# Kernel tuning notes

Hardware: AMD Instinct MI355X
Metric: run time of the kernel (lower is better)

## Reference

```python
import jax, jax.numpy as jnp
import numpy as np
import math

ALPHA_MIN = math.exp(-1.0 / 5.0)   # ~0.8187
ALPHA_MAX = math.exp(-1.0 / 25.0)  # ~0.9608
THRESHOLD = 1.0


def setup_inputs() -> dict:
    key = jax.random.key(0)
    k1, k2, k3, k4, k5 = jax.random.split(key, 5)
    B, T, I, H = 32, 2048, 256, 512
    x = jax.random.normal(k1, (B, T, I), dtype=jnp.float32)
    # Linear weight, kaiming-ish scale
    W = jax.random.normal(k2, (H, I), dtype=jnp.float32) * (1.0 / np.sqrt(I))
    # alpha ~ U[exp(-1/5), exp(-1/25)] as in nn.init.uniform_
    alpha = ALPHA_MIN + jax.random.uniform(k3, (H,), dtype=jnp.float32) * (ALPHA_MAX - ALPHA_MIN)
    # initial membrane potential / spike state (torch.rand in _lif_cell)
    u0 = jax.random.uniform(k4, (B, H), dtype=jnp.float32)
    s0 = jax.random.uniform(k5, (B, H), dtype=jnp.float32)
    return {"x": x, "W": W, "alpha": alpha, "u0": u0, "s0": s0}


def reference(x, W, alpha, u0, s0):
    # clamp alpha to its admissible range (lif_feature has no 'NoClamp')
    alpha = jnp.clip(alpha, ALPHA_MIN, ALPHA_MAX)
    b = 1.0 - alpha  # lif_feature has no 'B'

    # feedforward projection: [B, T, H]
    Wx = jnp.einsum('bti,hi->bth', x, W)

    def step(carry, wx_t):
        ut, st = carry
        ut = alpha * (ut - st) + b * wx_t          # leaky integrate + soft reset
        st = (ut - THRESHOLD > 0).astype(ut.dtype)  # heaviside spike
        return (ut, st), st

    # scan over time: Wx -> [T, B, H]
    _, s = jax.lax.scan(step, (u0, s0), jnp.swapaxes(Wx, 0, 1))
    return jnp.swapaxes(s, 0, 1)  # [B, T, H]
```

## Files before the change

kernel.cpp:

```cpp
#include <hip/hip_runtime.h>
#include <hip/hip_bf16.h>

#define ALPHA_MIN 0.8187307530779818f
#define ALPHA_MAX 0.9607894391523232f

typedef _Float16 f16;
typedef _Float16 f16x8 __attribute__((ext_vector_type(8)));
typedef float f32x16 __attribute__((ext_vector_type(16)));

#define LDSTRIDE 40

__global__ __launch_bounds__(256, 2) void gemm_fused(
    const float* __restrict__ X,
    const float* __restrict__ W,
    float* __restrict__ C,
    int M, int N, int K)
{
    __shared__ f16 Ah[2][128 * LDSTRIDE];
    __shared__ f16 Al[2][128 * LDSTRIDE];
    __shared__ f16 Bh[2][128 * LDSTRIDE];
    __shared__ f16 Bl[2][128 * LDSTRIDE];

    const int tid = threadIdx.x;
    const int mt = blockIdx.x >> 2;
    const int nt = blockIdx.x & 3;
    const int m0 = mt * 128, n0 = nt * 128;

    const int lane = tid & 63;
    const int wv   = tid >> 6;
    const int wm   = wv & 1;
    const int wn   = wv >> 1;
    const int fm   = lane & 31;
    const int fq   = lane >> 5;

    const int srow = tid >> 2;
    const int sc8  = tid & 3;

    const float* px0 = X + (size_t)(m0 + srow)      * K + sc8 * 8;
    const float* px1 = X + (size_t)(m0 + srow + 64) * K + sc8 * 8;
    const float* pw0 = W + (size_t)(n0 + srow)      * K + sc8 * 8;
    const float* pw1 = W + (size_t)(n0 + srow + 64) * K + sc8 * 8;

    f32x16 accH[2][2], accL[2][2];
#pragma unroll
    for (int i = 0; i < 2; ++i)
#pragma unroll
        for (int j = 0; j < 2; ++j)
#pragma unroll
            for (int e = 0; e < 16; ++e) { accH[i][j][e] = 0.0f; accL[i][j][e] = 0.0f; }

    float4 t[2][4];

    auto issue_loads = [&](int kt) {
        const int o = kt * 32;
        t[0][0] = *(const float4*)(px0 + o);
        t[0][1] = *(const float4*)(px0 + o + 4);
        t[0][2] = *(const float4*)(pw0 + o);
        t[0][3] = *(const float4*)(pw0 + o + 4);
        t[1][0] = *(const float4*)(px1 + o);
        t[1][1] = *(const float4*)(px1 + o + 4);
        t[1][2] = *(const float4*)(pw1 + o);
        t[1][3] = *(const float4*)(pw1 + o + 4);
    };

    auto write_lds = [&](int buf) {
#pragma unroll
        for (int i = 0; i < 2; ++i) {
            const int off = (srow + 64 * i) * LDSTRIDE + sc8 * 8;
            const float vx[8] = {t[i][0].x, t[i][0].y, t[i][0].z, t[i][0].w,
                                 t[i][1].x, t[i][1].y, t[i][1].z, t[i][1].w};
            const float vw[8] = {t[i][2].x, t[i][2].y, t[i][2].z, t[i][2].w,
                                 t[i][3].x, t[i][3].y, t[i][3].z, t[i][3].w};
            f16x8 xh, xl, wh, wl;
#pragma unroll
            for (int j = 0; j < 8; ++j) {
                const f16 hx = (f16)vx[j];
                xh[j] = hx; xl[j] = (f16)((vx[j] - (float)hx) * 2048.0f);
                const f16 hw = (f16)vw[j];
                wh[j] = hw; wl[j] = (f16)((vw[j] - (float)hw) * 2048.0f);
            }
            *(f16x8*)&Ah[buf][off] = xh;
            *(f16x8*)&Al[buf][off] = xl;
            *(f16x8*)&Bh[buf][off] = wh;
            *(f16x8*)&Bl[buf][off] = wl;
        }
    };

    const int KT = K / 32;
    issue_loads(0);
    write_lds(0);
    __syncthreads();

    for (int kt = 0; kt < KT; ++kt) {
        const int cur = kt & 1;
        if (kt + 1 < KT) issue_loads(kt + 1);

#pragma unroll
        for (int ks = 0; ks < 2; ++ks) {
            f16x8 af[2][2], bf[2][2];
#pragma unroll
            for (int mb = 0; mb < 2; ++mb) {
                const int ro = (wm * 64 + mb * 32 + fm) * LDSTRIDE + ks * 16 + fq * 8;
                af[mb][0] = *(const f16x8*)&Ah[cur][ro];
                af[mb][1] = *(const f16x8*)&Al[cur][ro];
            }
#pragma unroll
            for (int nb = 0; nb < 2; ++nb) {
                const int ro = (wn * 64 + nb * 32 + fm) * LDSTRIDE + ks * 16 + fq * 8;
                bf[nb][0] = *(const f16x8*)&Bh[cur][ro];
                bf[nb][1] = *(const f16x8*)&Bl[cur][ro];
            }
#pragma unroll
            for (int mb = 0; mb < 2; ++mb)
#pragma unroll
                for (int nb = 0; nb < 2; ++nb) {
                    accH[mb][nb] = __builtin_amdgcn_mfma_f32_32x32x16_f16(af[mb][0], bf[nb][0], accH[mb][nb], 0, 0, 0);
                    accL[mb][nb] = __builtin_amdgcn_mfma_f32_32x32x16_f16(af[mb][0], bf[nb][1], accL[mb][nb], 0, 0, 0);
                    accL[mb][nb] = __builtin_amdgcn_mfma_f32_32x32x16_f16(af[mb][1], bf[nb][0], accL[mb][nb], 0, 0, 0);
                }
        }

        if (kt + 1 < KT) write_lds(cur ^ 1);
        __syncthreads();
    }

#pragma unroll
    for (int mb = 0; mb < 2; ++mb)
#pragma unroll
        for (int nb = 0; nb < 2; ++nb) {
            const int col   = n0 + wn * 64 + nb * 32 + fm;
            const int rbase = m0 + wm * 64 + mb * 32 + 4 * fq;
#pragma unroll
            for (int g = 0; g < 4; ++g)
#pragma unroll
                for (int r = 0; r < 4; ++r) {
                    const int row = rbase + 8 * g + r;
                    C[(size_t)row * N + col] = accH[mb][nb][4 * g + r]
                                             + accL[mb][nb][4 * g + r] * (1.0f / 2048.0f);
                }
        }
}

#define SU 64

__global__ __launch_bounds__(64) void lif_scan2(
    const float* __restrict__ wx,
    float* __restrict__ out,
    const float* __restrict__ alpha,
    const float* __restrict__ u0,
    const float* __restrict__ s0,
    int T, int H)
{
    const int chain = blockIdx.x * 64 + threadIdx.x;
    const int h = chain % H;
    const int b = chain / H;

    float a = alpha[h];
    a = fminf(fmaxf(a, ALPHA_MIN), ALPHA_MAX);
    const float bb = 1.0f - a;

    float u = u0[chain];
    float s = s0[chain];

    const float* src = wx + (size_t)b * T * H + h;
    float* dst = out + (size_t)b * T * H + h;

    float w0[SU], w1[SU];
#pragma unroll
    for (int j = 0; j < SU; ++j) w0[j] = src[(size_t)j * H];

    const int NC = T / SU;
    for (int c = 0; c < NC; c += 2) {
#pragma unroll
        for (int j = 0; j < SU; ++j) w1[j] = src[(size_t)((c + 1) * SU + j) * H];
#pragma unroll
        for (int j = 0; j < SU; ++j) {
            u = fmaf(a, u - s, bb * w0[j]);
            s = (u > 1.0f) ? 1.0f : 0.0f;
            __builtin_nontemporal_store(s, &dst[(size_t)(c * SU + j) * H]);
        }
        if (c + 2 < NC) {
#pragma unroll
            for (int j = 0; j < SU; ++j) w0[j] = src[(size_t)((c + 2) * SU + j) * H];
        }
#pragma unroll
        for (int j = 0; j < SU; ++j) {
            u = fmaf(a, u - s, bb * w1[j]);
            s = (u > 1.0f) ? 1.0f : 0.0f;
            __builtin_nontemporal_store(s, &dst[(size_t)((c + 1) * SU + j) * H]);
        }
    }
}

__global__ __launch_bounds__(64) void lif_scan_inplace(
    float* __restrict__ buf, const float* __restrict__ alpha,
    const float* __restrict__ u0, const float* __restrict__ s0, int T, int H)
{
    const int chain = blockIdx.x * 64 + threadIdx.x;
    const int h = chain % H;
    const int b = chain / H;
    float a = alpha[h];
    a = fminf(fmaxf(a, ALPHA_MIN), ALPHA_MAX);
    const float bb = 1.0f - a;
    float u = u0[chain], s = s0[chain];
    float* base = buf + (size_t)b * T * H + h;
    for (int t0 = 0; t0 < T; t0 += 32) {
        float w[32];
#pragma unroll
        for (int j = 0; j < 32; ++j) w[j] = base[(size_t)(t0 + j) * H];
#pragma unroll
        for (int j = 0; j < 32; ++j) {
            u = fmaf(a, u - s, bb * w[j]);
            s = (u > 1.0f) ? 1.0f : 0.0f;
            base[(size_t)(t0 + j) * H] = s;
        }
    }
}

extern "C" void kernel_launch(void* const* d_in, const int* in_sizes, int n_in,
                              void* d_out, int out_size, void* d_ws, size_t ws_size,
                              hipStream_t stream) {
    const float* x     = (const float*)d_in[0];
    const float* W     = (const float*)d_in[1];
    const float* alpha = (const float*)d_in[2];
    const float* u0    = (const float*)d_in[3];
    const float* s0    = (const float*)d_in[4];
    float* out = (float*)d_out;

    const int H = in_sizes[2];
    const int I = in_sizes[1] / H;
    const int B = in_sizes[3] / H;
    const int T = in_sizes[0] / (B * I);
    const int M = B * T;

    const size_t szWx = (size_t)M * H * sizeof(float);

    if (ws_size >= szWx) {
        float* Wx = (float*)d_ws;
        gemm_fused<<<(M / 128) * (H / 128), 256, 0, stream>>>(x, W, Wx, M, H, I);
        lif_scan2<<<(B * H) / 64, 64, 0, stream>>>(Wx, out, alpha, u0, s0, T, H);
    } else {
        gemm_fused<<<(M / 128) * (H / 128), 256, 0, stream>>>(x, W, out, M, H, I);
        lif_scan_inplace<<<(B * H) / 64, 64, 0, stream>>>(out, alpha, u0, s0, T, H);
    }
}
```

Before: 302.3 us.

## Load raw fp32 tiles via global_load_lds and split to fp16 after LDS reads

Replaces the register-staged double-buffered fp16 hi/lo LDS tiles with direct global-to-LDS fp32 loads (global_load_lds) into XOR-swizzled buffers. The fp16 hi/lo split now happens after each LDS read, so every wave redoes it per fragment. This removes the register staging and the conversion-then-store step, and shrinks LDS use. The cost is losing the overlap of the next tile's load with compute: there is a single buffer with a sync before and after each k-step. It also adds a naive fallback GEMM for shapes other than the hardcoded ones.

```diff
diff --git a/kernel.cpp b/kernel.cpp
--- a/kernel.cpp
+++ b/kernel.cpp
@@ -1,5 +1,4 @@
 #include <hip/hip_runtime.h>
-#include <hip/hip_bf16.h>
 
 #define ALPHA_MIN 0.8187307530779818f
 #define ALPHA_MAX 0.9607894391523232f
@@ -8,18 +7,36 @@
 typedef _Float16 f16x8 __attribute__((ext_vector_type(8)));
 typedef float f32x16 __attribute__((ext_vector_type(16)));
 
-#define LDSTRIDE 40
-
-__global__ __launch_bounds__(256, 2) void gemm_fused(
+#define BB_ 32
+#define TT_ 2048
+#define KK_ 256
+#define HH_ 512
+
+__device__ __forceinline__ void gll16(const float* g, float* l) {
+    __builtin_amdgcn_global_load_lds(
+        (const __attribute__((address_space(1))) void*)g,
+        (__attribute__((address_space(3))) void*)l, 16, 0, 0);
+}
+
+__device__ __forceinline__ void cvt8(const float4 v0, const float4 v1,
+                                     f16x8& h, f16x8& l) {
+    const float v[8] = {v0.x, v0.y, v0.z, v0.w, v1.x, v1.y, v1.z, v1.w};
+#pragma unroll
+    for (int j = 0; j < 8; ++j) {
+        const f16 hj = (f16)v[j];
+        h[j] = hj;
+        l[j] = (f16)((v[j] - (float)hj) * 2048.0f);
+    }
+}
+
+__global__ __launch_bounds__(256) void gemm_lds(
     const float* __restrict__ X,
     const float* __restrict__ W,
     float* __restrict__ C,
     int M, int N, int K)
 {
-    __shared__ f16 Ah[2][128 * LDSTRIDE];
-    __shared__ f16 Al[2][128 * LDSTRIDE];
-    __shared__ f16 Bh[2][128 * LDSTRIDE];
-    __shared__ f16 Bl[2][128 * LDSTRIDE];
+    __shared__ float As[128 * 32];
+    __shared__ float Bs[128 * 32];
 
     const int tid = threadIdx.x;
     const int mt = blockIdx.x >> 2;
@@ -33,13 +50,9 @@
     const int fm   = lane & 31;
     const int fq   = lane >> 5;
 
-    const int srow = tid >> 2;
-    const int sc8  = tid & 3;
-
-    const float* px0 = X + (size_t)(m0 + srow)      * K + sc8 * 8;
-    const float* px1 = X + (size_t)(m0 + srow + 64) * K + sc8 * 8;
-    const float* pw0 = W + (size_t)(n0 + srow)      * K + sc8 * 8;
-    const float* pw1 = W + (size_t)(n0 + srow + 64) * K + sc8 * 8;
+    const int rA  = lane >> 3;
+    const int gq  = lane & 7;
+    const int gsw = gq ^ rA;
 
     f32x16 accH[2][2], accL[2][2];
 #pragma unroll
@@ -49,78 +62,47 @@
 #pragma unroll
             for (int e = 0; e < 16; ++e) { accH[i][j][e] = 0.0f; accL[i][j][e] = 0.0f; }
 
-    float4 t[2][4];
-
-    auto issue_loads = [&](int kt) {
-        const int o = kt * 32;
-        t[0][0] = *(const float4*)(px0 + o);
-        t[0][1] = *(const float4*)(px0 + o + 4);
-        t[0][2] = *(const float4*)(pw0 + o);
-        t[0][3] = *(const float4*)(pw0 + o + 4);
-        t[1][0] = *(const float4*)(px1 + o);
-        t[1][1] = *(const float4*)(px1 + o + 4);
-        t[1][2] = *(const float4*)(pw1 + o);
-        t[1][3] = *(const float4*)(pw1 + o + 4);
-    };
-
-    auto write_lds = [&](int buf) {
-#pragma unroll
-        for (int i = 0; i < 2; ++i) {
-            const int off = (srow + 64 * i) * LDSTRIDE + sc8 * 8;
-            const float vx[8] = {t[i][0].x, t[i][0].y, t[i][0].z, t[i][0].w,
-                                 t[i][1].x, t[i][1].y, t[i][1].z, t[i][1].w};
-            const float vw[8] = {t[i][2].x, t[i][2].y, t[i][2].z, t[i][2].w,
-                                 t[i][3].x, t[i][3].y, t[i][3].z, t[i][3].w};
-            f16x8 xh, xl, wh, wl;
-#pragma unroll
-            for (int j = 0; j < 8; ++j) {
-                const f16 hx = (f16)vx[j];
-                xh[j] = hx; xl[j] = (f16)((vx[j] - (float)hx) * 2048.0f);
-                const f16 hw = (f16)vw[j];
-                wh[j] = hw; wl[j] = (f16)((vw[j] - (float)hw) * 2048.0f);
+    const int KT = K / 32;
+    for (int kt = 0; kt < KT; ++kt) {
+#pragma unroll
+        for (int j = 0; j < 4; ++j) {
+            const int row = wv * 32 + j * 8 + rA;
+            gll16(&X[(size_t)(m0 + row) * K + kt * 32 + gsw * 4],
+                  &As[(wv * 32 + j * 8) * 32]);
+            gll16(&W[(size_t)(n0 + row) * K + kt * 32 + gsw * 4],
+                  &Bs[(wv * 32 + j * 8) * 32]);
+        }
+        __syncthreads();
+
+#pragma unroll
+        for (int ks = 0; ks < 2; ++ks) {
+            const int G = ks * 4 + fq * 2;
+            f16x8 ah[2], al[2], bh[2], bl[2];
+#pragma unroll
+            for (int mb = 0; mb < 2; ++mb) {
+                const int row = wm * 64 + mb * 32 + fm;
+                const int r7 = row & 7;
+                const float4 a0 = *(const float4*)&As[row * 32 + ((G    ) ^ r7) * 4];
+                const float4 a1 = *(const float4*)&As[row * 32 + ((G + 1) ^ r7) * 4];
+                cvt8(a0, a1, ah[mb], al[mb]);
             }
-            *(f16x8*)&Ah[buf][off] = xh;
-            *(f16x8*)&Al[buf][off] = xl;
-            *(f16x8*)&Bh[buf][off] = wh;
-            *(f16x8*)&Bl[buf][off] = wl;
-        }
-    };
-
-    const int KT = K / 32;
-    issue_loads(0);
-    write_lds(0);
-    __syncthreads();
-
-    for (int kt = 0; kt < KT; ++kt) {
-        const int cur = kt & 1;
-        if (kt + 1 < KT) issue_loads(kt + 1);
-
-#pragma unroll
-        for (int ks = 0; ks < 2; ++ks) {
-            f16x8 af[2][2], bf[2][2];
-#pragma unroll
-            for (int mb = 0; mb < 2; ++mb) {
-                const int ro = (wm * 64 + mb * 32 + fm) * LDSTRIDE + ks * 16 + fq * 8;
-                af[mb][0] = *(const f16x8*)&Ah[cur][ro];
-                af[mb][1] = *(const f16x8*)&Al[cur][ro];
+#pragma unroll
+            for (int nb = 0; nb < 2; ++nb) {
+                const int row = wn * 64 + nb * 32 + fm;
+                const int r7 = row & 7;
+                const float4 b0 = *(const float4*)&Bs[row * 32 + ((G    ) ^ r7) * 4];
+                const float4 b1 = *(const float4*)&Bs[row * 32 + ((G + 1) ^ r7) * 4];
+                cvt8(b0, b1, bh[nb], bl[nb]);
             }
 #pragma unroll
-            for (int nb = 0; nb < 2; ++nb) {
-                const int ro = (wn * 64 + nb * 32 + fm) * LDSTRIDE + ks * 16 + fq * 8;
-                bf[nb][0] = *(const f16x8*)&Bh[cur][ro];
-                bf[nb][1] = *(const f16x8*)&Bl[cur][ro];
-            }
-#pragma unroll
             for (int mb = 0; mb < 2; ++mb)
 #pragma unroll
                 for (int nb = 0; nb < 2; ++nb) {
-                    accH[mb][nb] = __builtin_amdgcn_mfma_f32_32x32x16_f16(af[mb][0], bf[nb][0], accH[mb][nb], 0, 0, 0);
-                    accL[mb][nb] = __builtin_amdgcn_mfma_f32_32x32x16_f16(af[mb][0], bf[nb][1], accL[mb][nb], 0, 0, 0);
-                    accL[mb][nb] = __builtin_amdgcn_mfma_f32_32x32x16_f16(af[mb][1], bf[nb][0], accL[mb][nb], 0, 0, 0);
+                    accH[mb][nb] = __builtin_amdgcn_mfma_f32_32x32x16_f16(ah[mb], bh[nb], accH[mb][nb], 0, 0, 0);
+                    accL[mb][nb] = __builtin_amdgcn_mfma_f32_32x32x16_f16(ah[mb], bl[nb], accL[mb][nb], 0, 0, 0);
+                    accL[mb][nb] = __builtin_amdgcn_mfma_f32_32x32x16_f16(al[mb], bh[nb], accL[mb][nb], 0, 0, 0);
                 }
         }
-
-        if (kt + 1 < KT) write_lds(cur ^ 1);
         __syncthreads();
     }
 
@@ -190,6 +172,17 @@
             __builtin_nontemporal_store(s, &dst[(size_t)((c + 1) * SU + j) * H]);
         }
     }
+}
+
+__global__ void gemm_naive(const float* __restrict__ X, const float* __restrict__ W,
+                           float* __restrict__ C, int M, int N, int K)
+{
+    const int idx = blockIdx.x * 256 + threadIdx.x;
+    if (idx >= M * N) return;
+    const int m = idx / N, n = idx % N;
+    float acc = 0.0f;
+    for (int k = 0; k < K; ++k) acc = fmaf(X[(size_t)m * K + k], W[(size_t)n * K + k], acc);
+    C[idx] = acc;
 }
 
 __global__ __launch_bounds__(64) void lif_scan_inplace(
@@ -204,16 +197,10 @@
     const float bb = 1.0f - a;
     float u = u0[chain], s = s0[chain];
     float* base = buf + (size_t)b * T * H + h;
-    for (int t0 = 0; t0 < T; t0 += 32) {
-        float w[32];
-#pragma unroll
-        for (int j = 0; j < 32; ++j) w[j] = base[(size_t)(t0 + j) * H];
-#pragma unroll
-        for (int j = 0; j < 32; ++j) {
-            u = fmaf(a, u - s, bb * w[j]);
-            s = (u > 1.0f) ? 1.0f : 0.0f;
-            base[(size_t)(t0 + j) * H] = s;
-        }
+    for (int t = 0; t < T; ++t) {
+        u = fmaf(a, u - s, bb * base[(size_t)t * H]);
+        s = (u > 1.0f) ? 1.0f : 0.0f;
+        base[(size_t)t * H] = s;
     }
 }
 
@@ -235,12 +222,12 @@
 
     const size_t szWx = (size_t)M * H * sizeof(float);
 
-    if (ws_size >= szWx) {
+    if (B == BB_ && T == TT_ && I == KK_ && H == HH_ && ws_size >= szWx) {
         float* Wx = (float*)d_ws;
-        gemm_fused<<<(M / 128) * (H / 128), 256, 0, stream>>>(x, W, Wx, M, H, I);
+        gemm_lds<<<(M / 128) * (H / 128), 256, 0, stream>>>(x, W, Wx, M, H, I);
         lif_scan2<<<(B * H) / 64, 64, 0, stream>>>(Wx, out, alpha, u0, s0, T, H);
     } else {
-        gemm_fused<<<(M / 128) * (H / 128), 256, 0, stream>>>(x, W, out, M, H, I);
-        lif_scan_inplace<<<(B * H) / 64, 64, 0, stream>>>(out, alpha, u0, s0, T, H);
-    }
-}
+        gemm_naive<<<(M * H + 255) / 256, 256, 0, stream>>>(x, W, out, M, H, I);
+        lif_scan_inplace<<<(B * H + 63) / 64, 64, 0, stream>>>(out, alpha, u0, s0, T, H);
+    }
+}
```

Result: slower. 373.1 us (+23.4%).
